# Optimization experiments

Measured on AMD Instinct MI355X. Metric: run time of the kernel, lower is better.

## Reference

```python
import jax, jax.numpy as jnp
import numpy as np

N_NODES = 50000
N_EDGES = 800000
D = 128


def setup_inputs() -> dict:
    key = jax.random.key(0)
    ks = jax.random.split(key, 6)
    x = jax.random.normal(ks[0], (N_NODES, D), dtype=jnp.float32)
    edge_index = jax.random.randint(ks[1], (2, N_EDGES), 0, N_NODES, dtype=jnp.int32)
    scale = 1.0 / np.sqrt(D)
    W0 = jax.random.normal(ks[2], (D, D), dtype=jnp.float32) * scale
    W1 = jax.random.normal(ks[3], (D, D), dtype=jnp.float32) * scale
    W2 = jax.random.normal(ks[4], (D, D), dtype=jnp.float32) * scale
    b0 = jnp.zeros((D,), jnp.float32)
    b1 = jnp.zeros((D,), jnp.float32)
    b2 = jnp.zeros((D,), jnp.float32)
    return {"x": x, "edge_index": edge_index, "W0": W0, "b0": b0,
            "W1": W1, "b1": b1, "W2": W2, "b2": b2}


def _gcn_norm(edge_index, n_nodes, dtype):
    # symmetric normalization D^-1/2 A D^-1/2, no self loops (add_self_loops=False)
    src, dst = edge_index[1], edge_index[0]  # adj_t: aggregate src -> dst
    deg = jax.ops.segment_sum(jnp.ones(src.shape, dtype), src, num_segments=n_nodes)
    dis = jnp.where(deg > 0, jax.lax.rsqrt(jnp.maximum(deg, 1.0)), 0.0)
    return src, dst, dis[src] * dis[dst]  # per-edge norm [E]


def _gcn_layer(x, W, b, src, dst, norm, n_nodes):
    h = x @ W                                   # [N, d_out]
    msg = h[src] * norm[:, None]                # gather + scale, [E, d_out]
    agg = jax.ops.segment_sum(msg, dst, num_segments=n_nodes)
    return agg + b


def reference(x, edge_index, W0, b0, W1, b1, W2, b2):
    n = x.shape[0]
    src, dst, norm = _gcn_norm(edge_index, n, x.dtype)
    h = jax.nn.relu(_gcn_layer(x, W0, b0, src, dst, norm, n))
    h = jax.nn.relu(_gcn_layer(h, W1, b1, src, dst, norm, n))
    return _gcn_layer(h, W2, b2, src, dst, norm, n)
```

## Files before the change

kernel.cpp:

```cpp
#include <hip/hip_runtime.h>
#include <hip/hip_bf16.h>

#define DFEAT 128
#define RSPLIT 8
#define SSPLIT 64

typedef __attribute__((ext_vector_type(8))) short short8;
typedef __attribute__((ext_vector_type(4))) float f32x4;

__device__ __forceinline__ ushort f2bf(float f) {
    uint u = __float_as_uint(f);
    u += 0x7FFF + ((u >> 16) & 1);
    return (ushort)(u >> 16);
}
__device__ __forceinline__ float bf_lo(uint v) { return __uint_as_float(v << 16); }
__device__ __forceinline__ float bf_hi(uint v) { return __uint_as_float(v & 0xFFFF0000u); }


__global__ __launch_bounds__(512) void histrank_kernel(const int* __restrict__ EI,
                                                       int* __restrict__ cnt_part,
                                                       int* __restrict__ deg_part,
                                                       int* __restrict__ erank,
                                                       int nedges, int nnodes,
                                                       int range, int slice) {
    extern __shared__ int lds[];
    int* hd = lds;
    int* hs = lds + range;
    const int r = blockIdx.x & (RSPLIT - 1);
    const int s = blockIdx.x / RSPLIT;
    const int base = r * range;
    for (int i = threadIdx.x; i < 2 * range; i += 512) lds[i] = 0;
    __syncthreads();

    const int e0 = s * slice;
    const int e1 = min(nedges, e0 + slice);
    for (int e = e0 + threadIdx.x; e < e1; e += 512) {
        int dst = EI[e];
        int src = EI[nedges + e];
        unsigned ud = (unsigned)(dst - base);
        unsigned us = (unsigned)(src - base);
        if (ud < (unsigned)range) erank[e] = atomicAdd(&hd[ud], 1);
        if (us < (unsigned)range) atomicAdd(&hs[us], 1);
    }
    __syncthreads();

    for (int i = threadIdx.x; i < range; i += 512) {
        int node = base + i;
        if (node < nnodes) {
            cnt_part[s * nnodes + node] = hd[i];
            deg_part[s * nnodes + node] = hs[i];
        }
    }
}

__global__ __launch_bounds__(1024) void scan1_kernel(int* __restrict__ cnt_part,
                                                     const int* __restrict__ deg_part,
                                                     int* __restrict__ offs,
                                                     int* __restrict__ bsums,
                                                     float* __restrict__ dis, int n) {
    __shared__ int sm[1024];
    int t = threadIdx.x;
    int g = blockIdx.x * 1024 + t;
    int c = 0;
    if (g < n) {
        int d = 0;
        #pragma unroll
        for (int s = 0; s < SSPLIT; ++s) {
            int v = cnt_part[s * n + g];
            cnt_part[s * n + g] = c;
            c += v;
            d += deg_part[s * n + g];
        }
        dis[g] = (d > 0) ? rsqrtf((float)d) : 0.0f;
    }
    sm[t] = c;
    __syncthreads();
    for (int off = 1; off < 1024; off <<= 1) {
        int add = (t >= off) ? sm[t - off] : 0;
        __syncthreads();
        sm[t] += add;
        __syncthreads();
    }
    if (g < n) offs[g + 1] = sm[t];
    if (t == 1023) bsums[blockIdx.x] = sm[1023];
}

__global__ __launch_bounds__(1024) void scan3_kernel(int* __restrict__ offs,
                                                     const int* __restrict__ bsums,
                                                     int n, int nb) {
    __shared__ int pre[64];
    int t = threadIdx.x;
    if (t < 64) {
        int v = (t < nb) ? bsums[t] : 0;
        for (int off = 1; off < 64; off <<= 1) {
            int u = __shfl_up(v, off);
            if (t >= off) v += u;
        }
        int ex = __shfl_up(v, 1);
        if (t == 0) ex = 0;
        pre[t] = ex;
    }
    __syncthreads();
    int add = pre[blockIdx.x];
    int g = blockIdx.x * 1024 + t;
    if (g < n) offs[g + 1] += add;
    if (blockIdx.x == 0 && t == 0) offs[0] = 0;
}

__global__ void fill_kernel(const int* __restrict__ EI, const int* __restrict__ offs,
                            const int* __restrict__ erank, const int* __restrict__ sprefix,
                            int* __restrict__ esrc, int nedges, int nnodes, int slice) {
    int e = blockIdx.x * blockDim.x + threadIdx.x;
    if (e >= nedges) return;
    int dst = EI[e];
    int src = EI[nedges + e];
    int s = e / slice;
    int idx = offs[dst] + sprefix[s * nnodes + dst] + erank[e];
    esrc[idx] = src;
}

__global__ void prepw_kernel(const float* __restrict__ W0, const float* __restrict__ W1,
                             const float* __restrict__ W2, ushort* __restrict__ Wtb) {
    int i = blockIdx.x * 256 + threadIdx.x;
    int m = i >> 14, r = i & 16383;
    int n = r >> 7, k = r & 127;
    const float* W = (m == 0) ? W0 : (m == 1) ? W1 : W2;
    Wtb[i] = f2bf(W[k * DFEAT + n]);
}


template <int IN_F32>
__global__ __launch_bounds__(256) void gemm_mfma(const void* __restrict__ Xin,
                                                 const ushort* __restrict__ Wtb,
                                                 const float* __restrict__ dis,
                                                 ushort* __restrict__ Hb, int nrows) {
    __shared__ ushort wlds[128 * 136];
    const int t = threadIdx.x;

    #pragma unroll
    for (int q = 0; q < 8; ++q) {
        int c = t + q * 256;
        int row = c >> 4, cr = c & 15;
        short8 v = *(const short8*)(Wtb + c * 8);
        *(short8*)(&wlds[row * 136 + cr * 8]) = v;
    }

    const int lane = t & 63;
    const int r16 = lane & 15, g = lane >> 4;
    const int wv = t >> 6;
    const int rbase = blockIdx.x * 128 + wv * 16;

    short8 a[2][4];
    #pragma unroll
    for (int rt = 0; rt < 2; ++rt) {
        int row = rbase + rt * 64 + r16;
        int srow = (row < nrows) ? row : (nrows - 1);
        if (IN_F32) {
            const float* X = (const float*)Xin;
            #pragma unroll
            for (int kc = 0; kc < 4; ++kc) {
                const float* p = X + (size_t)srow * DFEAT + kc * 32 + g * 8;
                float4 f0 = *(const float4*)p;
                float4 f1 = *(const float4*)(p + 4);
                short8 sv;
                sv[0] = (short)f2bf(f0.x); sv[1] = (short)f2bf(f0.y);
                sv[2] = (short)f2bf(f0.z); sv[3] = (short)f2bf(f0.w);
                sv[4] = (short)f2bf(f1.x); sv[5] = (short)f2bf(f1.y);
                sv[6] = (short)f2bf(f1.z); sv[7] = (short)f2bf(f1.w);
                a[rt][kc] = sv;
            }
        } else {
            const ushort* X = (const ushort*)Xin;
            #pragma unroll
            for (int kc = 0; kc < 4; ++kc)
                a[rt][kc] = *(const short8*)(X + (size_t)srow * DFEAT + kc * 32 + g * 8);
        }
    }
    __syncthreads();

    f32x4 acc[2][8];
    #pragma unroll
    for (int rt = 0; rt < 2; ++rt)
        #pragma unroll
        for (int nt = 0; nt < 8; ++nt) acc[rt][nt] = (f32x4){0.f, 0.f, 0.f, 0.f};

    #pragma unroll
    for (int kc = 0; kc < 4; ++kc) {
        #pragma unroll
        for (int nt = 0; nt < 8; ++nt) {
            short8 b = *(const short8*)(&wlds[(nt * 16 + r16) * 136 + kc * 32 + g * 8]);
            acc[0][nt] = __builtin_amdgcn_mfma_f32_16x16x32_bf16(a[0][kc], b, acc[0][nt], 0, 0, 0);
            acc[1][nt] = __builtin_amdgcn_mfma_f32_16x16x32_bf16(a[1][kc], b, acc[1][nt], 0, 0, 0);
        }
    }

    #pragma unroll
    for (int rt = 0; rt < 2; ++rt) {
        const int orow_base = rbase + rt * 64 + g * 4;
        #pragma unroll
        for (int r = 0; r < 4; ++r) {
            int orow = orow_base + r;
            if (orow < nrows) {
                float d = dis[orow];
                #pragma unroll
                for (int nt = 0; nt < 8; ++nt)
                    Hb[(size_t)orow * DFEAT + nt * 16 + r16] = f2bf(acc[rt][nt][r] * d);
            }
        }
    }
}


template <int RELU, int OUT_F32>
__global__ __launch_bounds__(256) void agg_kernel(const ushort* __restrict__ H,
                                                  const int* __restrict__ offs,
                                                  const int* __restrict__ esrc,
                                                  const float* __restrict__ dis,
                                                  const float* __restrict__ bias,
                                                  void* __restrict__ OUT, int nnodes) {
    int node = blockIdx.x * 4 + (threadIdx.x >> 6);
    if (node >= nnodes) return;
    int lane = threadIdx.x & 63;
    int q = lane >> 4;
    int l16 = lane & 15;
    int s = offs[node];
    int deg = offs[node + 1] - s;

    float a0 = 0.f, a1 = 0.f, a2 = 0.f, a3 = 0.f;
    float a4 = 0.f, a5 = 0.f, a6 = 0.f, a7 = 0.f;
    float c0 = 0.f, c1 = 0.f, c2 = 0.f, c3 = 0.f;
    float c4 = 0.f, c5 = 0.f, c6 = 0.f, c7 = 0.f;
    const ushort* __restrict__ Hp = H + l16 * 8;

    for (int base = 0; base < deg; base += 64) {
        int rem = deg - base;
        int cnt = (rem < 64) ? rem : 64;
        int idx = (base + lane < deg) ? esrc[s + base + lane] : 0;
        int clen = (cnt + 3) >> 2;
        int jbase = q * clen;
        for (int jj = 0; jj < clen; jj += 2) {
            int j0 = jbase + jj;
            int j1 = jbase + jj + 1;
            int s0 = __shfl(idx, j0 & 63);
            int s1 = __shfl(idx, j1 & 63);
            float m0 = (j0 < cnt) ? 1.f : 0.f;
            float m1 = ((jj + 1 < clen) && (j1 < cnt)) ? 1.f : 0.f;
            uint4 v0 = *(const uint4*)(Hp + (size_t)s0 * DFEAT);
            uint4 v1 = *(const uint4*)(Hp + (size_t)s1 * DFEAT);
            a0 = fmaf(m0, bf_lo(v0.x), a0); a1 = fmaf(m0, bf_hi(v0.x), a1);
            a2 = fmaf(m0, bf_lo(v0.y), a2); a3 = fmaf(m0, bf_hi(v0.y), a3);
            a4 = fmaf(m0, bf_lo(v0.z), a4); a5 = fmaf(m0, bf_hi(v0.z), a5);
            a6 = fmaf(m0, bf_lo(v0.w), a6); a7 = fmaf(m0, bf_hi(v0.w), a7);
            c0 = fmaf(m1, bf_lo(v1.x), c0); c1 = fmaf(m1, bf_hi(v1.x), c1);
            c2 = fmaf(m1, bf_lo(v1.y), c2); c3 = fmaf(m1, bf_hi(v1.y), c3);
            c4 = fmaf(m1, bf_lo(v1.z), c4); c5 = fmaf(m1, bf_hi(v1.z), c5);
            c6 = fmaf(m1, bf_lo(v1.w), c6); c7 = fmaf(m1, bf_hi(v1.w), c7);
        }
    }
    a0 += c0; a1 += c1; a2 += c2; a3 += c3;
    a4 += c4; a5 += c5; a6 += c6; a7 += c7;

    a0 += __shfl_xor(a0, 16); a1 += __shfl_xor(a1, 16);
    a2 += __shfl_xor(a2, 16); a3 += __shfl_xor(a3, 16);
    a4 += __shfl_xor(a4, 16); a5 += __shfl_xor(a5, 16);
    a6 += __shfl_xor(a6, 16); a7 += __shfl_xor(a7, 16);
    a0 += __shfl_xor(a0, 32); a1 += __shfl_xor(a1, 32);
    a2 += __shfl_xor(a2, 32); a3 += __shfl_xor(a3, 32);
    a4 += __shfl_xor(a4, 32); a5 += __shfl_xor(a5, 32);
    a6 += __shfl_xor(a6, 32); a7 += __shfl_xor(a7, 32);

    float dn = dis[node];
    float4 b0 = *(const float4*)&bias[l16 * 8];
    float4 b1 = *(const float4*)&bias[l16 * 8 + 4];
    float r0 = dn * a0 + b0.x, r1 = dn * a1 + b0.y;
    float r2 = dn * a2 + b0.z, r3 = dn * a3 + b0.w;
    float r4 = dn * a4 + b1.x, r5 = dn * a5 + b1.y;
    float r6 = dn * a6 + b1.z, r7 = dn * a7 + b1.w;
    if (RELU) {
        r0 = fmaxf(r0, 0.f); r1 = fmaxf(r1, 0.f);
        r2 = fmaxf(r2, 0.f); r3 = fmaxf(r3, 0.f);
        r4 = fmaxf(r4, 0.f); r5 = fmaxf(r5, 0.f);
        r6 = fmaxf(r6, 0.f); r7 = fmaxf(r7, 0.f);
    }
    if (q == 0) {
        if (OUT_F32) {
            float* o = (float*)OUT + (size_t)node * DFEAT + l16 * 8;
            *(float4*)o = make_float4(r0, r1, r2, r3);
            *(float4*)(o + 4) = make_float4(r4, r5, r6, r7);
        } else {
            uint4 p;
            p.x = (uint)f2bf(r0) | ((uint)f2bf(r1) << 16);
            p.y = (uint)f2bf(r2) | ((uint)f2bf(r3) << 16);
            p.z = (uint)f2bf(r4) | ((uint)f2bf(r5) << 16);
            p.w = (uint)f2bf(r6) | ((uint)f2bf(r7) << 16);
            *(uint4*)((ushort*)OUT + (size_t)node * DFEAT + l16 * 8) = p;
        }
    }
}


extern "C" void kernel_launch(void* const* d_in, const int* in_sizes, int n_in,
                              void* d_out, int out_size, void* d_ws, size_t ws_size,
                              hipStream_t stream) {
    const float* x  = (const float*)d_in[0];
    const int*   EI = (const int*)d_in[1];
    const float* W0 = (const float*)d_in[2];
    const float* b0 = (const float*)d_in[3];
    const float* W1 = (const float*)d_in[4];
    const float* b1 = (const float*)d_in[5];
    const float* W2 = (const float*)d_in[6];
    const float* b2 = (const float*)d_in[7];
    float* out = (float*)d_out;

    const int N = in_sizes[0] / DFEAT;
    const int E = in_sizes[1] / 2;
    const int range = (N + RSPLIT - 1) / RSPLIT;
    const int slice = (E + SSPLIT - 1) / SSPLIT;

    char* w = (char*)d_ws;
    auto alloc = [&](size_t bytes) {
        void* p = (void*)w;
        w += (bytes + 255) & ~(size_t)255;
        return p;
    };
    int*    offs  = (int*)alloc((size_t)(N + 1) * 4);
    int*    bsums = (int*)alloc(64 * 4);
    float*  dis   = (float*)alloc((size_t)N * 4);
    int*    erank = (int*)alloc((size_t)E * 4);
    int*    esrc  = (int*)alloc((size_t)E * 4);
    ushort* Wtb   = (ushort*)alloc((size_t)3 * DFEAT * DFEAT * 2);
    ushort* hbuf  = (ushort*)alloc((size_t)N * DFEAT * 2);
    ushort* abuf  = (ushort*)alloc((size_t)N * DFEAT * 2);

    int* cnt_part = (int*)hbuf;
    int* deg_part = (int*)abuf;

    const int nb = (N + 1023) / 1024;

    prepw_kernel<<<(3 * DFEAT * DFEAT) / 256, 256, 0, stream>>>(W0, W1, W2, Wtb);
    histrank_kernel<<<RSPLIT * SSPLIT, 512, 2 * range * 4, stream>>>(
        EI, cnt_part, deg_part, erank, E, N, range, slice);
    scan1_kernel<<<nb, 1024, 0, stream>>>(cnt_part, deg_part, offs, bsums, dis, N);
    scan3_kernel<<<nb, 1024, 0, stream>>>(offs, bsums, N, nb);
    fill_kernel<<<(E + 255) / 256, 256, 0, stream>>>(EI, offs, erank, cnt_part,
                                                     esrc, E, N, slice);

    const int gemmGrid = (N + 127) / 128;
    const int aggGrid  = (N + 3) / 4;

    gemm_mfma<1><<<gemmGrid, 256, 0, stream>>>(x, Wtb, dis, hbuf, N);
    agg_kernel<1, 0><<<aggGrid, 256, 0, stream>>>(hbuf, offs, esrc, dis, b0, abuf, N);
    gemm_mfma<0><<<gemmGrid, 256, 0, stream>>>(abuf, Wtb + DFEAT * DFEAT, dis, hbuf, N);
    agg_kernel<1, 0><<<aggGrid, 256, 0, stream>>>(hbuf, offs, esrc, dis, b1, abuf, N);
    gemm_mfma<0><<<gemmGrid, 256, 0, stream>>>(abuf, Wtb + 2 * DFEAT * DFEAT, dis, hbuf, N);
    agg_kernel<0, 1><<<aggGrid, 256, 0, stream>>>(hbuf, offs, esrc, dis, b2, out, N);
}
```

Measured before the change: 198.4 us.

## Fold weight prep into histogram kernel, narrow counters to 16-bit, unroll gather 4x

The separate weight-transpose/bf16 kernel is merged into the histogram kernel: 512 blocks with 96 threads each cover the 49152 weight elements, which saves one launch. The per-slice counts, degrees and edge ranks are stored as 16-bit values, halving the traffic through scan1 and fill. The aggregation inner loop now issues four row gathers per iteration instead of two, giving more memory-level parallelism. The 16-bit fields assume per-slice counts and prefixes stay below 65536, which holds for this input size. The unrolled loop reads shuffle lanes past the chunk end, and those lanes are masked out.

```diff
diff --git a/kernel.cpp b/kernel.cpp
--- a/kernel.cpp
+++ b/kernel.cpp
@@ -18,9 +18,13 @@
 
 
 __global__ __launch_bounds__(512) void histrank_kernel(const int* __restrict__ EI,
-                                                       int* __restrict__ cnt_part,
-                                                       int* __restrict__ deg_part,
-                                                       int* __restrict__ erank,
+                                                       ushort* __restrict__ cnt_part,
+                                                       ushort* __restrict__ deg_part,
+                                                       ushort* __restrict__ erank,
+                                                       const float* __restrict__ W0,
+                                                       const float* __restrict__ W1,
+                                                       const float* __restrict__ W2,
+                                                       ushort* __restrict__ Wtb,
                                                        int nedges, int nnodes,
                                                        int range, int slice) {
     extern __shared__ int lds[];
@@ -29,6 +33,15 @@
     const int r = blockIdx.x & (RSPLIT - 1);
     const int s = blockIdx.x / RSPLIT;
     const int base = r * range;
+
+    if (threadIdx.x < 96) {
+        int i = blockIdx.x * 96 + threadIdx.x;
+        int m = i >> 14, rr = i & 16383;
+        int n = rr >> 7, k = rr & 127;
+        const float* W = (m == 0) ? W0 : (m == 1) ? W1 : W2;
+        Wtb[i] = f2bf(W[k * DFEAT + n]);
+    }
+
     for (int i = threadIdx.x; i < 2 * range; i += 512) lds[i] = 0;
     __syncthreads();
 
@@ -39,7 +52,7 @@
         int src = EI[nedges + e];
         unsigned ud = (unsigned)(dst - base);
         unsigned us = (unsigned)(src - base);
-        if (ud < (unsigned)range) erank[e] = atomicAdd(&hd[ud], 1);
+        if (ud < (unsigned)range) erank[e] = (ushort)atomicAdd(&hd[ud], 1);
         if (us < (unsigned)range) atomicAdd(&hs[us], 1);
     }
     __syncthreads();
@@ -47,14 +60,14 @@
     for (int i = threadIdx.x; i < range; i += 512) {
         int node = base + i;
         if (node < nnodes) {
-            cnt_part[s * nnodes + node] = hd[i];
-            deg_part[s * nnodes + node] = hs[i];
-        }
-    }
-}
-
-__global__ __launch_bounds__(1024) void scan1_kernel(int* __restrict__ cnt_part,
-                                                     const int* __restrict__ deg_part,
+            cnt_part[s * nnodes + node] = (ushort)hd[i];
+            deg_part[s * nnodes + node] = (ushort)hs[i];
+        }
+    }
+}
+
+__global__ __launch_bounds__(1024) void scan1_kernel(ushort* __restrict__ cnt_part,
+                                                     const ushort* __restrict__ deg_part,
                                                      int* __restrict__ offs,
                                                      int* __restrict__ bsums,
                                                      float* __restrict__ dis, int n) {
@@ -67,7 +80,7 @@
         #pragma unroll
         for (int s = 0; s < SSPLIT; ++s) {
             int v = cnt_part[s * n + g];
-            cnt_part[s * n + g] = c;
+            cnt_part[s * n + g] = (ushort)c;
             c += v;
             d += deg_part[s * n + g];
         }
@@ -108,24 +121,16 @@
 }
 
 __global__ void fill_kernel(const int* __restrict__ EI, const int* __restrict__ offs,
-                            const int* __restrict__ erank, const int* __restrict__ sprefix,
+                            const ushort* __restrict__ erank,
+                            const ushort* __restrict__ sprefix,
                             int* __restrict__ esrc, int nedges, int nnodes, int slice) {
     int e = blockIdx.x * blockDim.x + threadIdx.x;
     if (e >= nedges) return;
     int dst = EI[e];
     int src = EI[nedges + e];
     int s = e / slice;
-    int idx = offs[dst] + sprefix[s * nnodes + dst] + erank[e];
+    int idx = offs[dst] + (int)sprefix[s * nnodes + dst] + (int)erank[e];
     esrc[idx] = src;
-}
-
-__global__ void prepw_kernel(const float* __restrict__ W0, const float* __restrict__ W1,
-                             const float* __restrict__ W2, ushort* __restrict__ Wtb) {
-    int i = blockIdx.x * 256 + threadIdx.x;
-    int m = i >> 14, r = i & 16383;
-    int n = r >> 7, k = r & 127;
-    const float* W = (m == 0) ? W0 : (m == 1) ? W1 : W2;
-    Wtb[i] = f2bf(W[k * DFEAT + n]);
 }
 
 
@@ -238,15 +243,20 @@
         int idx = (base + lane < deg) ? esrc[s + base + lane] : 0;
         int clen = (cnt + 3) >> 2;
         int jbase = q * clen;
-        for (int jj = 0; jj < clen; jj += 2) {
+        for (int jj = 0; jj < clen; jj += 4) {
             int j0 = jbase + jj;
-            int j1 = jbase + jj + 1;
-            int s0 = __shfl(idx, j0 & 63);
-            int s1 = __shfl(idx, j1 & 63);
+            int s0 = __shfl(idx, j0);
+            int s1 = __shfl(idx, j0 + 1);
+            int s2 = __shfl(idx, j0 + 2);
+            int s3 = __shfl(idx, j0 + 3);
             float m0 = (j0 < cnt) ? 1.f : 0.f;
-            float m1 = ((jj + 1 < clen) && (j1 < cnt)) ? 1.f : 0.f;
+            float m1 = ((jj + 1 < clen) && (j0 + 1 < cnt)) ? 1.f : 0.f;
+            float m2 = ((jj + 2 < clen) && (j0 + 2 < cnt)) ? 1.f : 0.f;
+            float m3 = ((jj + 3 < clen) && (j0 + 3 < cnt)) ? 1.f : 0.f;
             uint4 v0 = *(const uint4*)(Hp + (size_t)s0 * DFEAT);
             uint4 v1 = *(const uint4*)(Hp + (size_t)s1 * DFEAT);
+            uint4 v2 = *(const uint4*)(Hp + (size_t)s2 * DFEAT);
+            uint4 v3 = *(const uint4*)(Hp + (size_t)s3 * DFEAT);
             a0 = fmaf(m0, bf_lo(v0.x), a0); a1 = fmaf(m0, bf_hi(v0.x), a1);
             a2 = fmaf(m0, bf_lo(v0.y), a2); a3 = fmaf(m0, bf_hi(v0.y), a3);
             a4 = fmaf(m0, bf_lo(v0.z), a4); a5 = fmaf(m0, bf_hi(v0.z), a5);
@@ -255,6 +265,14 @@
             c2 = fmaf(m1, bf_lo(v1.y), c2); c3 = fmaf(m1, bf_hi(v1.y), c3);
             c4 = fmaf(m1, bf_lo(v1.z), c4); c5 = fmaf(m1, bf_hi(v1.z), c5);
             c6 = fmaf(m1, bf_lo(v1.w), c6); c7 = fmaf(m1, bf_hi(v1.w), c7);
+            a0 = fmaf(m2, bf_lo(v2.x), a0); a1 = fmaf(m2, bf_hi(v2.x), a1);
+            a2 = fmaf(m2, bf_lo(v2.y), a2); a3 = fmaf(m2, bf_hi(v2.y), a3);
+            a4 = fmaf(m2, bf_lo(v2.z), a4); a5 = fmaf(m2, bf_hi(v2.z), a5);
+            a6 = fmaf(m2, bf_lo(v2.w), a6); a7 = fmaf(m2, bf_hi(v2.w), a7);
+            c0 = fmaf(m3, bf_lo(v3.x), c0); c1 = fmaf(m3, bf_hi(v3.x), c1);
+            c2 = fmaf(m3, bf_lo(v3.y), c2); c3 = fmaf(m3, bf_hi(v3.y), c3);
+            c4 = fmaf(m3, bf_lo(v3.z), c4); c5 = fmaf(m3, bf_hi(v3.z), c5);
+            c6 = fmaf(m3, bf_lo(v3.w), c6); c7 = fmaf(m3, bf_hi(v3.w), c7);
         }
     }
     a0 += c0; a1 += c1; a2 += c2; a3 += c3;
@@ -326,20 +344,19 @@
     int*    offs  = (int*)alloc((size_t)(N + 1) * 4);
     int*    bsums = (int*)alloc(64 * 4);
     float*  dis   = (float*)alloc((size_t)N * 4);
-    int*    erank = (int*)alloc((size_t)E * 4);
+    ushort* erank = (ushort*)alloc((size_t)E * 2);
     int*    esrc  = (int*)alloc((size_t)E * 4);
     ushort* Wtb   = (ushort*)alloc((size_t)3 * DFEAT * DFEAT * 2);
     ushort* hbuf  = (ushort*)alloc((size_t)N * DFEAT * 2);
     ushort* abuf  = (ushort*)alloc((size_t)N * DFEAT * 2);
 
-    int* cnt_part = (int*)hbuf;
-    int* deg_part = (int*)abuf;
+    ushort* cnt_part = (ushort*)hbuf;
+    ushort* deg_part = (ushort*)abuf;
 
     const int nb = (N + 1023) / 1024;
 
-    prepw_kernel<<<(3 * DFEAT * DFEAT) / 256, 256, 0, stream>>>(W0, W1, W2, Wtb);
     histrank_kernel<<<RSPLIT * SSPLIT, 512, 2 * range * 4, stream>>>(
-        EI, cnt_part, deg_part, erank, E, N, range, slice);
+        EI, cnt_part, deg_part, erank, W0, W1, W2, Wtb, E, N, range, slice);
     scan1_kernel<<<nb, 1024, 0, stream>>>(cnt_part, deg_part, offs, bsums, dis, N);
     scan3_kernel<<<nb, 1024, 0, stream>>>(offs, bsums, N, nb);
     fill_kernel<<<(E + 255) / 256, 256, 0, stream>>>(EI, offs, erank, cnt_part,
```

Result: faster. 188.1 us, median of 2 (-5.2%).
